# Kernel tuning notes

Hardware: AMD Instinct MI355X
Metric: run time of the kernel (lower is better)

## Reference

```python
import jax, jax.numpy as jnp
import numpy as np

EPS = 1e-5

def _hdc_branch(emb, w, b, dil, ln_g, ln_b):
    # emb: [N, L, E]; w: [K, E, F] ('WIO'); same-length dilated conv
    y = jax.lax.conv_general_dilated(
        emb, w, window_strides=(1,), padding=[(dil, dil)],
        rhs_dilation=(dil,), dimension_numbers=('NWC', 'WIO', 'NWC')) + b
    m = y.mean(-1, keepdims=True)
    v = ((y - m) ** 2).mean(-1, keepdims=True)
    y = (y - m) / jnp.sqrt(v + EPS) * ln_g + ln_b
    return jax.nn.relu(y)  # [N, L, F]

def _news_encoder(titles, embedding, w1, b1, w2, b2, w3, b3, ln_g, ln_b,
                  q_levels, q_words):
    B, n, L = titles.shape
    E = embedding.shape[-1]
    emb = embedding[titles].reshape(B * n, L, E)  # dropout = identity (eval)
    d = jnp.stack([
        _hdc_branch(emb, w1, b1, 1, ln_g, ln_b),
        _hdc_branch(emb, w2, b2, 2, ln_g, ln_b),
        _hdc_branch(emb, w3, b3, 3, ln_g, ln_b),
    ], axis=2)  # [Bn, L, 3, F]
    F = d.shape[-1]
    d = d.reshape(B, n, L, 3, F)
    scale = jnp.sqrt(jnp.asarray(E, d.dtype))  # original divides by sqrt(embedding_dim)
    # level-wise attention pooling (1-row query over 3 levels)
    wl = jax.nn.softmax(jnp.einsum('f,bnlkf->bnlk', q_levels[0], d) / scale, axis=-1)
    attn = jnp.einsum('bnlk,bnlkf->bnlf', wl, d)  # [B, n, L, F]
    # word-wise attention pooling (1-row query over L words)
    ww = jax.nn.softmax(jnp.einsum('f,bnlf->bnl', q_words[0], attn) / scale, axis=-1)
    reprs = jnp.einsum('bnl,bnlf->bnf', ww, attn)  # [B, n, F]
    return reprs

def setup_inputs() -> dict:
    key = jax.random.key(0)
    ks = jax.random.split(key, 12)
    V, E, F, H = 50000, 300, 150, 50
    return {
        'candidate_title': jax.random.randint(ks[0], (64, 5, 30), 0, V),
        'clicked_title': jax.random.randint(ks[1], (64, H, 30), 0, V),
        'embedding': jax.random.normal(ks[2], (V, E), jnp.float32),
        'w1': jax.random.normal(ks[3], (3, E, F), jnp.float32) * 0.05,
        'b1': jax.random.normal(ks[4], (F,), jnp.float32) * 0.05,
        'w2': jax.random.normal(ks[5], (3, E, F), jnp.float32) * 0.05,
        'b2': jax.random.normal(ks[6], (F,), jnp.float32) * 0.05,
        'w3': jax.random.normal(ks[7], (3, E, F), jnp.float32) * 0.05,
        'b3': jax.random.normal(ks[8], (F,), jnp.float32) * 0.05,
        'ln_g': jnp.ones((F,), jnp.float32),
        'ln_b': jnp.zeros((F,), jnp.float32),
        'q_levels': jax.random.normal(ks[9], (1, F), jnp.float32),
        'q_words': jax.random.normal(ks[10], (1, F), jnp.float32),
        'ltr_w': jax.random.normal(ks[11], (1, H), jnp.float32) * 0.1,
        'ltr_b': jnp.zeros((1,), jnp.float32),
    }

def reference(candidate_title, clicked_title, embedding, w1, b1, w2, b2, w3, b3,
              ln_g, ln_b, q_levels, q_words, ltr_w, ltr_b):
    cdd = _news_encoder(candidate_title, embedding, w1, b1, w2, b2, w3, b3,
                        ln_g, ln_b, q_levels, q_words)  # [B, cdd, F]
    his = _news_encoder(clicked_title, embedding, w1, b1, w2, b2, w3, b3,
                        ln_g, ln_b, q_levels, q_words)  # [B, his, F]
    scores = jnp.einsum('bcf,bhf->bch', cdd, his)        # [B, cdd, his]
    logits = jnp.einsum('bch,oh->bco', scores, ltr_w)[..., 0] + ltr_b[0]  # [B, cdd]
    return jax.nn.log_softmax(logits, axis=1)  # cdd_size > 1 branch
```

## Files before the change

kernel.cpp:

```cpp
#include <hip/hip_runtime.h>

typedef unsigned short u16;
typedef unsigned int   u32;
typedef __bf16 bf16x8 __attribute__((ext_vector_type(8)));
typedef float  f32x4  __attribute__((ext_vector_type(4)));
typedef _Float16 h2 __attribute__((ext_vector_type(2)));

#define M_ROWS 50000
#define M_PAD  50176
#define M_TILES 196
#define N_REAL 1368
#define N_PAD  1536
#define N_TILES 11
#define K_DIM  300
#define K_PAD  320
#define KT     10
#define TROW   1408
#define SEG    152
#define YCOL   152
#define TS     136

#define GLDS(gp, lp) __builtin_amdgcn_global_load_lds( \
    (const __attribute__((address_space(1))) void*)(gp), \
    (__attribute__((address_space(3))) void*)(lp), 16, 0, 0)

static __device__ __forceinline__ u16 f2bf(float x){
  union { float f; u32 u; } a; a.f = x;
  u32 r = a.u + 0x7fffu + ((a.u >> 16) & 1u);
  return (u16)(r >> 16);
}
static __device__ __forceinline__ u16 f2h(float x){
  _Float16 h = (_Float16)x;
  u16 r; __builtin_memcpy(&r, &h, 2); return r;
}
static __device__ __forceinline__ float h2f(u16 v){
  _Float16 h; __builtin_memcpy(&h, &v, 2); return (float)h;
}

static __device__ __forceinline__ float wsum63(float x){
  asm volatile(
    "s_nop 1\n\t"
    "v_add_f32 %0, %0, %0 row_shr:1 bound_ctrl:0\n\t"
    "s_nop 1\n\t"
    "v_add_f32 %0, %0, %0 row_shr:2 bound_ctrl:0\n\t"
    "s_nop 1\n\t"
    "v_add_f32 %0, %0, %0 row_shr:4 bound_ctrl:0\n\t"
    "s_nop 1\n\t"
    "v_add_f32 %0, %0, %0 row_shr:8 bound_ctrl:0\n\t"
    "s_nop 1\n\t"
    "v_add_f32 %0, %0, %0 row_bcast:15 row_mask:0xa\n\t"
    "s_nop 1\n\t"
    "v_add_f32 %0, %0, %0 row_bcast:31 row_mask:0xc\n\t"
    "s_nop 1"
    : "+v"(x));
  return x;
}
static __device__ __forceinline__ float wmax63(float x){
  asm volatile(
    "s_nop 1\n\t"
    "v_max_f32 %0, %0, %0 row_shr:1\n\t"
    "s_nop 1\n\t"
    "v_max_f32 %0, %0, %0 row_shr:2\n\t"
    "s_nop 1\n\t"
    "v_max_f32 %0, %0, %0 row_shr:4\n\t"
    "s_nop 1\n\t"
    "v_max_f32 %0, %0, %0 row_shr:8\n\t"
    "s_nop 1\n\t"
    "v_max_f32 %0, %0, %0 row_bcast:15 row_mask:0xa\n\t"
    "s_nop 1\n\t"
    "v_max_f32 %0, %0, %0 row_bcast:31 row_mask:0xc\n\t"
    "s_nop 1"
    : "+v"(x));
  return x;
}
static __device__ __forceinline__ float rdl63(float x){
  union { float f; int i; } a; a.f = x;
  union { int i; float f; } r; r.i = __builtin_amdgcn_readlane(a.i, 63);
  return r.f;
}

__global__ __launch_bounds__(256) void build_A(const float* __restrict__ emb, u16* __restrict__ A){
  int t = blockIdx.x * 256 + threadIdx.x;
  if (t >= M_PAD * 40) return;
  int m = t / 40, kg = t % 40;
  int k0 = kg * 8;
  int kt = kg >> 2, kgl = kg & 3;
  int tile = m >> 8, ml = m & 255, mb = ml >> 4, row = ml & 15;
  size_t off = ((size_t)tile * KT + kt) * 8192 + mb * 512 + kgl * 128 + row * 8;
  union { uint4 q; u16 s[8]; } p;
  if (m < M_ROWS && k0 + 8 <= K_DIM){
    const float4* src = (const float4*)(emb + (size_t)m * K_DIM + k0);
    float4 v0 = src[0], v1 = src[1];
    p.s[0] = f2bf(v0.x); p.s[1] = f2bf(v0.y); p.s[2] = f2bf(v0.z); p.s[3] = f2bf(v0.w);
    p.s[4] = f2bf(v1.x); p.s[5] = f2bf(v1.y); p.s[6] = f2bf(v1.z); p.s[7] = f2bf(v1.w);
  } else {
    #pragma unroll
    for (int j = 0; j < 8; ++j){
      int k = k0 + j;
      float x = (m < M_ROWS && k < K_DIM) ? emb[(size_t)m * K_DIM + k] : 0.f;
      p.s[j] = f2bf(x);
    }
  }
  *(uint4*)(A + off) = p.q;
}

__global__ void build_B(const float* __restrict__ w1, const float* __restrict__ w2,
                        const float* __restrict__ w3, u16* __restrict__ B){
  int t = blockIdx.x * 256 + threadIdx.x;
  if (t >= N_PAD * K_PAD) return;
  int n = t / K_PAD, k = t % K_PAD;
  float x = 0.f;
  if (n < N_REAL && k < K_DIM){
    int br = n / 456, rem = n % 456, tap = rem / 152, f = rem % 152;
    if (f < 150){
      const float* w = (br == 0) ? w1 : ((br == 1) ? w2 : w3);
      x = w[(tap * K_DIM + k) * 150 + f];
    }
  }
  int tn = n >> 7, nl = n & 127, nb = nl >> 4, col = nl & 15;
  int kt = k >> 5, kl = k & 31, kg = kl >> 3, k8 = kl & 7;
  B[((size_t)tn * KT + kt) * 4096 + nb * 512 + kg * 128 + col * 8 + k8] = f2bf(x);
}

__global__ __launch_bounds__(512, 4) void gemm_k(const u16* __restrict__ A, const u16* __restrict__ B,
                                                 u16* __restrict__ T){
  __shared__ __align__(16) u16 lds[24576];
  u16* lA = lds;
  u16* lB = lds + 16384;
  const int tn = blockIdx.x, tileM = blockIdx.y;
  const int tid = threadIdx.x, wave = tid >> 6, lane = tid & 63;
  const int wm = wave >> 1, wn = wave & 1;
  f32x4 acc[4][4];
  #pragma unroll
  for (int i = 0; i < 4; ++i)
    #pragma unroll
    for (int j = 0; j < 4; ++j) acc[i][j] = (f32x4){0.f, 0.f, 0.f, 0.f};
  const u16* Ab = A + (size_t)tileM * KT * 8192;
  const u16* Bb = B + (size_t)tn * KT * 4096;
  for (int rd = 0; rd < 5; ++rd){
    __syncthreads();
    #pragma unroll
    for (int j = 0; j < 4; ++j)
      GLDS(Ab + rd * 16384 + j * 4096 + tid * 8, lA + j * 4096 + tid * 8);
    #pragma unroll
    for (int j = 0; j < 2; ++j)
      GLDS(Bb + rd * 8192 + j * 4096 + tid * 8, lB + j * 4096 + tid * 8);
    __syncthreads();
    #pragma unroll
    for (int kk = 0; kk < 2; ++kk){
      const bf16x8* A8 = (const bf16x8*)(lA + kk * 8192);
      const bf16x8* B8 = (const bf16x8*)(lB + kk * 4096);
      bf16x8 av[4], bv[4];
      #pragma unroll
      for (int i = 0; i < 4; ++i) av[i] = A8[(wm * 4 + i) * 64 + lane];
      #pragma unroll
      for (int j = 0; j < 4; ++j) bv[j] = B8[(wn * 4 + j) * 64 + lane];
      #pragma unroll
      for (int i = 0; i < 4; ++i)
        #pragma unroll
        for (int j = 0; j < 4; ++j)
          acc[i][j] = __builtin_amdgcn_mfma_f32_16x16x32_bf16(av[i], bv[j], acc[i][j], 0, 0, 0);
    }
  }
  const int r0 = (lane >> 4) * 4, c0 = lane & 15;
  const int row = tid >> 2, q = tid & 3;
  #pragma unroll
  for (int half = 0; half < 2; ++half){
    __syncthreads();
    if ((wm >> 1) == half){
      const int rbase = (wm & 1) * 64;
      #pragma unroll
      for (int i = 0; i < 4; ++i){
        #pragma unroll
        for (int j = 0; j < 4; ++j){
          int col = wn * 64 + j * 16 + c0;
          #pragma unroll
          for (int r = 0; r < 4; ++r)
            lds[(rbase + i * 16 + r0 + r) * TS + col] = f2h(acc[i][j][r]);
        }
      }
    }
    __syncthreads();
    int m = tileM * 256 + half * 128 + row;
    if (m < M_ROWS){
      const u16* src = lds + row * TS + q * 32;
      u16* dst = T + (size_t)m * TROW + tn * 128 + q * 32;
      uint4 v0 = *(const uint4*)(src);
      uint4 v1 = *(const uint4*)(src + 8);
      uint4 v2 = *(const uint4*)(src + 16);
      uint4 v3 = *(const uint4*)(src + 24);
      *(uint4*)(dst)      = v0;
      *(uint4*)(dst + 8)  = v1;
      *(uint4*)(dst + 16) = v2;
      *(uint4*)(dst + 24) = v3;
    }
  }
}

__global__ __launch_bounds__(512, 8) void encode_k(
    const int* __restrict__ cand, const int* __restrict__ clk,
    const u16* __restrict__ T,
    const float* __restrict__ b1, const float* __restrict__ b2, const float* __restrict__ b3,
    const float* __restrict__ lng, const float* __restrict__ lnb,
    const float* __restrict__ ql, const float* __restrict__ qw,
    float* __restrict__ rc, float* __restrict__ rh){
  __shared__ __align__(16) u16 ybuf[90][YCOL];
  __shared__ float tl[32];
  __shared__ float pbuf[8][YCOL];
  __shared__ u32 wordoff[30];
  const int t = blockIdx.x;
  const int tid = threadIdx.x, wave = tid >> 6, lane = tid & 63;
  const int* wp; float* outp;
  if (t < 320){ wp = cand + t * 30;                outp = rc + t * 150; }
  else        { wp = clk + (size_t)(t - 320) * 30; outp = rh + (size_t)(t - 320) * 150; }
  if (tid < 30) wordoff[tid] = (u32)wp[tid] * (u32)TROW;
  __syncthreads();
  const float invs = 0.057735026918962576f;
  const int f0 = lane, f1 = lane + 64, f2 = lane + 128;
  const bool has2 = (f2 < 150);

  #pragma unroll
  for (int it = 0; it < 4; ++it){
    int item = tid + it * 512;
    if (item < 1710){
      int p = item / 19, fg = item - p * 19;
      int l = p / 3, br = p - l * 3, dil = br + 1;
      union { uint4 q; h2 h[4]; } s; s.q = (uint4){0u, 0u, 0u, 0u};
      #pragma unroll
      for (int tap = 0; tap < 3; ++tap){
        int ls = l + (tap - 1) * dil;
        if (ls >= 0 && ls < 30){
          union { uint4 q; h2 h[4]; } v;
          v.q = *(const uint4*)(T + wordoff[ls] + br * 456 + tap * SEG + fg * 8);
          #pragma unroll
          for (int i = 0; i < 4; ++i) s.h[i] += v.h[i];
        }
      }
      *(uint4*)&ybuf[p][fg * 8] = s.q;
    }
  }

  float qlv0 = ql[f0], qlv1 = ql[f1], qlv2 = has2 ? ql[f2] : 0.f;
  float qwv0 = qw[f0], qwv1 = qw[f1], qwv2 = has2 ? qw[f2] : 0.f;
  float lg0 = lng[f0], lg1 = lng[f1], lg2 = has2 ? lng[f2] : 0.f;
  float lb0 = lnb[f0], lb1 = lnb[f1], lb2 = has2 ? lnb[f2] : 0.f;
  float bs[3][3];
  {
    const float* bl[3] = {b1, b2, b3};
    #pragma unroll
    for (int br = 0; br < 3; ++br){
      bs[br][0] = bl[br][f0]; bs[br][1] = bl[br][f1]; bs[br][2] = has2 ? bl[br][f2] : 0.f;
    }
  }
  __syncthreads();

  float at0[4], at1[4], at2[4]; int myl[4]; int nw = 0;
  for (int l = wave; l < 30; l += 8){
    float dr[3][3]; float lvl[3];
    #pragma unroll
    for (int br = 0; br < 3; ++br){
      int p = l * 3 + br;
      float y0 = h2f(ybuf[p][f0]) + bs[br][0];
      float y1 = h2f(ybuf[p][f1]) + bs[br][1];
      float y2 = has2 ? (h2f(ybuf[p][f2]) + bs[br][2]) : 0.f;
      float s  = y0 + y1 + y2;
      float ss = y0 * y0 + y1 * y1 + y2 * y2;
      float st = wsum63(s), sst = wsum63(ss);
      float mean = rdl63(st) * (1.f / 150.f);
      float var  = rdl63(sst) * (1.f / 150.f) - mean * mean;
      float rstd = rsqrtf(var + 1e-5f);
      float d0 = fmaxf((y0 - mean) * rstd * lg0 + lb0, 0.f);
      float d1 = fmaxf((y1 - mean) * rstd * lg1 + lb1, 0.f);
      float d2 = has2 ? fmaxf((y2 - mean) * rstd * lg2 + lb2, 0.f) : 0.f;
      dr[br][0] = d0; dr[br][1] = d1; dr[br][2] = d2;
      float dot = qlv0 * d0 + qlv1 * d1 + qlv2 * d2;
      lvl[br] = rdl63(wsum63(dot)) * invs;
    }
    float mx = fmaxf(lvl[0], fmaxf(lvl[1], lvl[2]));
    float e0 = __expf(lvl[0] - mx), e1 = __expf(lvl[1] - mx), e2 = __expf(lvl[2] - mx);
    float inv = 1.f / (e0 + e1 + e2);
    float w0 = e0 * inv, w1v = e1 * inv, w2v = e2 * inv;
    float a0 = w0 * dr[0][0] + w1v * dr[1][0] + w2v * dr[2][0];
    float a1 = w0 * dr[0][1] + w1v * dr[1][1] + w2v * dr[2][1];
    float a2 = w0 * dr[0][2] + w1v * dr[1][2] + w2v * dr[2][2];
    float dot = qwv0 * a0 + qwv1 * a1 + qwv2 * a2;
    float tw = wsum63(dot);
    if (lane == 63) tl[l] = tw * invs;
    at0[nw] = a0; at1[nw] = a1; at2[nw] = a2; myl[nw] = l; ++nw;
  }
  __syncthreads();

  if (wave == 0){
    float v = (lane < 30) ? tl[lane] : -1e30f;
    float mx = rdl63(wmax63(v));
    float e = (lane < 30) ? __expf(v - mx) : 0.f;
    float den = rdl63(wsum63(e));
    if (lane < 30) tl[lane] = e / den;
  }
  __syncthreads();

  float p0 = 0.f, p1 = 0.f, p2 = 0.f;
  for (int q = 0; q < nw; ++q){
    float wwv = tl[myl[q]];
    p0 += wwv * at0[q]; p1 += wwv * at1[q]; p2 += wwv * at2[q];
  }
  pbuf[wave][lane] = p0;
  pbuf[wave][lane + 64] = p1;
  if (has2) pbuf[wave][lane + 128] = p2;
  __syncthreads();
  if (tid < 150){
    float acc = 0.f;
    #pragma unroll
    for (int w = 0; w < 8; ++w) acc += pbuf[w][tid];
    outp[tid] = acc;
  }
}

__global__ __launch_bounds__(256) void final_k(const float* __restrict__ rc, const float* __restrict__ rh,
                                               const float* __restrict__ lw, const float* __restrict__ lb,
                                               float* __restrict__ out){
  __shared__ float Cl[750];
  __shared__ float Hl[7500];
  __shared__ float sc[5][52];
  __shared__ float lg[5];
  const int b = blockIdx.x, tid = threadIdx.x;
  const float* C = rc + b * 750;
  const float* H = rh + (size_t)b * 7500;
  for (int i = tid; i < 750; i += 256) Cl[i] = C[i];
  for (int i = tid; i < 7500; i += 256) Hl[i] = H[i];
  __syncthreads();
  if (tid < 250){
    int c = tid / 50, h = tid % 50;
    float s = 0.f;
    #pragma unroll 10
    for (int k = 0; k < 150; ++k) s += Cl[c * 150 + k] * Hl[h * 150 + k];
    sc[c][h] = s;
  }
  __syncthreads();
  if (tid < 5){
    float s = lb[0];
    for (int h = 0; h < 50; ++h) s += sc[tid][h] * lw[h];
    lg[tid] = s;
  }
  __syncthreads();
  if (tid < 5){
    float mx = fmaxf(fmaxf(fmaxf(lg[0], lg[1]), fmaxf(lg[2], lg[3])), lg[4]);
    float den = 0.f;
    for (int c = 0; c < 5; ++c) den += expf(lg[c] - mx);
    out[b * 5 + tid] = lg[tid] - mx - logf(den);
  }
}

extern "C" void kernel_launch(void* const* d_in, const int* in_sizes, int n_in,
                              void* d_out, int out_size, void* d_ws, size_t ws_size,
                              hipStream_t stream){
  const int*   cand = (const int*)d_in[0];
  const int*   clk  = (const int*)d_in[1];
  const float* emb  = (const float*)d_in[2];
  const float* w1   = (const float*)d_in[3];
  const float* b1   = (const float*)d_in[4];
  const float* w2   = (const float*)d_in[5];
  const float* b2   = (const float*)d_in[6];
  const float* w3   = (const float*)d_in[7];
  const float* b3   = (const float*)d_in[8];
  const float* lng  = (const float*)d_in[9];
  const float* lnb  = (const float*)d_in[10];
  const float* ql   = (const float*)d_in[11];
  const float* qw   = (const float*)d_in[12];
  const float* lw   = (const float*)d_in[13];
  const float* lb   = (const float*)d_in[14];
  float* out = (float*)d_out;

  char* ws = (char*)d_ws;
  const size_t szA = (size_t)M_TILES * KT * 16384;
  const size_t szB = (size_t)12 * KT * 8192;
  const size_t szT = (size_t)M_ROWS * TROW * 2;
  u16*   A  = (u16*)ws;
  u16*   B  = (u16*)(ws + szA);
  u16*   T  = (u16*)(ws + szA + szB);
  float* rc = (float*)(ws + szA + szB + szT);
  float* rh = rc + 320 * 150;

  build_A<<<(M_PAD * 40 + 255) / 256, 256, 0, stream>>>(emb, A);
  build_B<<<(N_PAD * K_PAD + 255) / 256, 256, 0, stream>>>(w1, w2, w3, B);
  gemm_k<<<dim3(N_TILES, M_TILES), 512, 0, stream>>>(A, B, T);
  encode_k<<<3520, 512, 0, stream>>>(cand, clk, T, b1, b2, b3, lng, lnb, ql, qw, rc, rh);
  final_k<<<64, 256, 0, stream>>>(rc, rh, lw, lb, out);
}
```

Measured before the change: 299.2 us.

## Halve GEMM LDS staging, raise occupancy, and group-swizzle block order

```diff
diff --git a/kernel.cpp b/kernel.cpp
--- a/kernel.cpp
+++ b/kernel.cpp
@@ -122,12 +122,14 @@
   B[((size_t)tn * KT + kt) * 4096 + nb * 512 + kg * 128 + col * 8 + k8] = f2bf(x);
 }
 
-__global__ __launch_bounds__(512, 4) void gemm_k(const u16* __restrict__ A, const u16* __restrict__ B,
+__global__ __launch_bounds__(512, 8) void gemm_k(const u16* __restrict__ A, const u16* __restrict__ B,
                                                  u16* __restrict__ T){
-  __shared__ __align__(16) u16 lds[24576];
-  u16* lA = lds;
-  u16* lB = lds + 16384;
-  const int tn = blockIdx.x, tileM = blockIdx.y;
+  __shared__ __align__(16) u16 lds[12288];
+  const int bid = blockIdx.x;
+  const int grp = bid / 88, r88 = bid - grp * 88;
+  const int tileM = (r88 & 7) + 8 * grp;
+  const int tn = r88 >> 3;
+  if (tileM >= M_TILES) return;
   const int tid = threadIdx.x, wave = tid >> 6, lane = tid & 63;
   const int wm = wave >> 1, wn = wave & 1;
   f32x4 acc[4][4];
@@ -137,38 +139,31 @@
     for (int j = 0; j < 4; ++j) acc[i][j] = (f32x4){0.f, 0.f, 0.f, 0.f};
   const u16* Ab = A + (size_t)tileM * KT * 8192;
   const u16* Bb = B + (size_t)tn * KT * 4096;
-  for (int rd = 0; rd < 5; ++rd){
+  for (int rd = 0; rd < KT; ++rd){
     __syncthreads();
-    #pragma unroll
-    for (int j = 0; j < 4; ++j)
-      GLDS(Ab + rd * 16384 + j * 4096 + tid * 8, lA + j * 4096 + tid * 8);
-    #pragma unroll
-    for (int j = 0; j < 2; ++j)
-      GLDS(Bb + rd * 8192 + j * 4096 + tid * 8, lB + j * 4096 + tid * 8);
+    GLDS(Ab + rd * 8192 + tid * 8,        lds + tid * 8);
+    GLDS(Ab + rd * 8192 + 4096 + tid * 8, lds + 4096 + tid * 8);
+    GLDS(Bb + rd * 4096 + tid * 8,        lds + 8192 + tid * 8);
     __syncthreads();
-    #pragma unroll
-    for (int kk = 0; kk < 2; ++kk){
-      const bf16x8* A8 = (const bf16x8*)(lA + kk * 8192);
-      const bf16x8* B8 = (const bf16x8*)(lB + kk * 4096);
-      bf16x8 av[4], bv[4];
+    const bf16x8* A8 = (const bf16x8*)lds;
+    const bf16x8* B8 = (const bf16x8*)(lds + 8192);
+    bf16x8 av[4], bv[4];
+    #pragma unroll
+    for (int i = 0; i < 4; ++i) av[i] = A8[(wm * 4 + i) * 64 + lane];
+    #pragma unroll
+    for (int j = 0; j < 4; ++j) bv[j] = B8[(wn * 4 + j) * 64 + lane];
+    #pragma unroll
+    for (int i = 0; i < 4; ++i)
       #pragma unroll
-      for (int i = 0; i < 4; ++i) av[i] = A8[(wm * 4 + i) * 64 + lane];
-      #pragma unroll
-      for (int j = 0; j < 4; ++j) bv[j] = B8[(wn * 4 + j) * 64 + lane];
-      #pragma unroll
-      for (int i = 0; i < 4; ++i)
-        #pragma unroll
-        for (int j = 0; j < 4; ++j)
-          acc[i][j] = __builtin_amdgcn_mfma_f32_16x16x32_bf16(av[i], bv[j], acc[i][j], 0, 0, 0);
-    }
+      for (int j = 0; j < 4; ++j)
+        acc[i][j] = __builtin_amdgcn_mfma_f32_16x16x32_bf16(av[i], bv[j], acc[i][j], 0, 0, 0);
   }
   const int r0 = (lane >> 4) * 4, c0 = lane & 15;
-  const int row = tid >> 2, q = tid & 3;
+  const int row = tid >> 3, q = tid & 7;
   #pragma unroll
-  for (int half = 0; half < 2; ++half){
+  for (int p = 0; p < 4; ++p){
     __syncthreads();
-    if ((wm >> 1) == half){
-      const int rbase = (wm & 1) * 64;
+    if (wm == p){
       #pragma unroll
       for (int i = 0; i < 4; ++i){
         #pragma unroll
@@ -176,23 +171,19 @@
           int col = wn * 64 + j * 16 + c0;
           #pragma unroll
           for (int r = 0; r < 4; ++r)
-            lds[(rbase + i * 16 + r0 + r) * TS + col] = f2h(acc[i][j][r]);
+            lds[(i * 16 + r0 + r) * TS + col] = f2h(acc[i][j][r]);
         }
       }
     }
     __syncthreads();
-    int m = tileM * 256 + half * 128 + row;
+    int m = tileM * 256 + p * 64 + row;
     if (m < M_ROWS){
-      const u16* src = lds + row * TS + q * 32;
-      u16* dst = T + (size_t)m * TROW + tn * 128 + q * 32;
+      const u16* src = lds + row * TS + q * 16;
+      u16* dst = T + (size_t)m * TROW + tn * 128 + q * 16;
       uint4 v0 = *(const uint4*)(src);
       uint4 v1 = *(const uint4*)(src + 8);
-      uint4 v2 = *(const uint4*)(src + 16);
-      uint4 v3 = *(const uint4*)(src + 24);
-      *(uint4*)(dst)      = v0;
-      *(uint4*)(dst + 8)  = v1;
-      *(uint4*)(dst + 16) = v2;
-      *(uint4*)(dst + 24) = v3;
+      *(uint4*)(dst)     = v0;
+      *(uint4*)(dst + 8) = v1;
     }
   }
 }
@@ -383,7 +374,7 @@
 
   build_A<<<(M_PAD * 40 + 255) / 256, 256, 0, stream>>>(emb, A);
   build_B<<<(N_PAD * K_PAD + 255) / 256, 256, 0, stream>>>(w1, w2, w3, B);
-  gemm_k<<<dim3(N_TILES, M_TILES), 512, 0, stream>>>(A, B, T);
+  gemm_k<<<2200, 512, 0, stream>>>(A, B, T);
   encode_k<<<3520, 512, 0, stream>>>(cand, clk, T, b1, b2, b3, lng, lnb, ql, qw, rc, rh);
   final_k<<<64, 256, 0, stream>>>(rc, rh, lw, lb, out);
 }
```

After: 699.6 us. 2.34x slower.
